# Kernel optimization log

Measured on AMD Instinct MI355X. Metric: run time of the kernel, lower is better.

The kernel has to match this reference:

```python
import jax, jax.numpy as jnp
import numpy as np

N_NODES = 4096
N_EDGES = 65536
BS = 16
LEAKY_SLOPE = 0.01
BN_EPS = 1e-5


def _init(key, shape, scale=0.02):
    return (jax.random.normal(key, shape, dtype=jnp.float32) * scale)


def setup_inputs() -> dict:
    key = jax.random.key(0)
    ks = jax.random.split(key, 20)
    x_in = jax.random.normal(ks[0], (N_NODES, 8500), dtype=jnp.float32)
    edge_index = jax.random.randint(ks[1], (2, N_EDGES), 0, N_NODES, dtype=jnp.int64)
    return {
        "x_in": x_in,
        "edge_index": edge_index,
        # SAGEConv params: Wl (neighbor lin, with bias), Wr (root lin, no bias)
        "W1l": _init(ks[2], (320, 8500)), "b1": jnp.zeros((320,), jnp.float32), "W1r": _init(ks[3], (320, 8500)),
        "W2l": _init(ks[4], (180, 320)),  "b2": jnp.zeros((180,), jnp.float32), "W2r": _init(ks[5], (180, 320)),
        "W3l": _init(ks[6], (90, 180)),   "b3": jnp.zeros((90,), jnp.float32),  "W3r": _init(ks[7], (90, 180)),
        "W4l": _init(ks[8], (50, 90)),    "b4": jnp.zeros((50,), jnp.float32),  "W4r": _init(ks[9], (50, 90)),
        "Wf1": _init(ks[10], (32, 50)),   "bf1": jnp.zeros((32,), jnp.float32),
        "Wf2": _init(ks[11], (16, 32)),   "bf2": jnp.zeros((16,), jnp.float32),
        "Wf3": _init(ks[12], (1, 16)),    "bf3": jnp.zeros((1,), jnp.float32),
    }


def _sage(x, src, dst, Wl, bl, Wr):
    # PyG SAGEConv: out = lin_l(mean_{j in N(i)} x_j) + lin_r(x_i)
    agg = jax.ops.segment_sum(x[src], dst, num_segments=N_NODES)          # [N, F]
    deg = jax.ops.segment_sum(jnp.ones_like(dst, dtype=x.dtype), dst, num_segments=N_NODES)
    mean = agg / jnp.maximum(deg, 1.0)[:, None]
    return mean @ Wl.T + bl + x @ Wr.T


def _leaky(x):
    return jnp.where(x >= 0, x, LEAKY_SLOPE * x)


def _bn(x):
    # F.batch_norm(x, None, None, training=True): per-feature, biased var, no affine
    m = jnp.mean(x, axis=0)
    v = jnp.mean((x - m) ** 2, axis=0)
    return (x - m) / jnp.sqrt(v + BN_EPS)


def reference(x_in, edge_index,
              W1l, b1, W1r, W2l, b2, W2r, W3l, b3, W3r, W4l, b4, W4r,
              Wf1, bf1, Wf2, bf2, Wf3, bf3):
    src, dst = edge_index[0], edge_index[1]
    x = _bn(_leaky(_sage(x_in, src, dst, W1l, b1, W1r)))
    x = _bn(_leaky(_sage(x, src, dst, W2l, b2, W2r)))
    x = _bn(_leaky(_sage(x, src, dst, W3l, b3, W3r)))
    x = _bn(_leaky(_sage(x, src, dst, W4l, b4, W4r)))
    # get_batch: label i -> floor(i / (N/BS)); global_add_pool == segment sum
    x = x.reshape(BS, N_NODES // BS, -1).sum(axis=1)                      # [BS, 50]
    x = x @ Wf1.T + bf1
    x = x @ Wf2.T + bf2
    x = x @ Wf3.T + bf3
    return x
```

## Files before the change

### kernel.cpp

```cpp
#include <hip/hip_runtime.h>
#include <stdint.h>

#define NN 4096
#define NE 65536
#define LEAKY 0.01f
#define BN_EPS 1e-5f
#define DSTRIDE 96

typedef float f32x4 __attribute__((ext_vector_type(4)));
typedef __bf16 bf16x8 __attribute__((ext_vector_type(8)));
typedef unsigned short u16x8 __attribute__((ext_vector_type(8)));

static __device__ __forceinline__ unsigned short f2bf(float v) {
  unsigned int u = __float_as_uint(v);
  u += 0x7fff + ((u >> 16) & 1);
  return (unsigned short)(u >> 16);
}

typedef __attribute__((address_space(1))) void gvoid;
typedef __attribute__((address_space(3))) void lvoid;

static __device__ __forceinline__ void async16(const void* g, void* l) {
  __builtin_amdgcn_global_load_lds((gvoid*)(uintptr_t)g,
                                   (lvoid*)(uint32_t)(uintptr_t)l, 16, 0, 0);
}


static __device__ __forceinline__ void pack_w_seg(int lblk, const float* __restrict__ Wl,
                                                  const float* __restrict__ Wr,
                                                  unsigned short* __restrict__ dst,
                                                  int Fout, int Fin, int Kp, int Np) {
  int nb = Kp >> 3;
  int idx = lblk * 256 + threadIdx.x;
  if (idx >= Np * nb) return;
  int row = idx / nb, kb = idx - row * nb;
  int g = kb >> 3, b = kb & 7;
  int dkb = (g << 3) | ((b + row) & 7);
  const float* src = nullptr;
  if (row < Fout)          src = Wl + (size_t)row * Fin;
  else if (row < 2 * Fout) src = Wr + (size_t)(row - Fout) * Fin;
  u16x8 st;
#pragma unroll
  for (int o = 0; o < 8; ++o) {
    int k = kb * 8 + o;
    float v = (src && k < Fin) ? src[k] : 0.f;
    st[o] = f2bf(v);
  }
  *(u16x8*)&dst[(size_t)row * Kp + dkb * 8] = st;
}

static __device__ __forceinline__ void px_load(const float* __restrict__ x, int idx,
                                               float v[8]) {
  int row = idx / 1064, kb = idx - row * 1064;
  const float* src = x + (size_t)row * 8500 + kb * 8;
  if (kb < 1062) {
    f32x4 a = *(const f32x4*)src;
    f32x4 c = *(const f32x4*)(src + 4);
#pragma unroll
    for (int o = 0; o < 4; ++o) { v[o] = a[o]; v[o + 4] = c[o]; }
  } else {
#pragma unroll
    for (int o = 0; o < 8; ++o) {
      int k = kb * 8 + o;
      v[o] = (k < 8500) ? src[o] : 0.f;
    }
  }
}

static __device__ __forceinline__ void px_store(unsigned short* __restrict__ xbf, int idx,
                                                const float v[8]) {
  int row = idx / 1064, kb = idx - row * 1064;
  int g = kb >> 3, b = kb & 7;
  int dkb = (g << 3) | ((b + row) & 7);
  u16x8 st;
#pragma unroll
  for (int o = 0; o < 8; ++o) st[o] = f2bf(v[o]);
  *(u16x8*)&xbf[(size_t)row * 8512 + dkb * 8] = st;
}

#define ADJ_BLK    256
#define PX_HALF  2179072
#define PX_BLK     8512
#define PW1_BLK    2660
#define PW2_BLK      60
#define PW3_BLK      24
#define PW4_BLK       8
#define SETUP_BLK (ADJ_BLK + PX_BLK + PW1_BLK + PW2_BLK + PW3_BLK + PW4_BLK)

__global__ __launch_bounds__(256) void setup_all(
    const float* __restrict__ x, const int* __restrict__ esrc, const int* __restrict__ edst,
    const float* __restrict__ W1l, const float* __restrict__ W1r,
    const float* __restrict__ W2l, const float* __restrict__ W2r,
    const float* __restrict__ W3l, const float* __restrict__ W3r,
    const float* __restrict__ W4l, const float* __restrict__ W4r,
    unsigned short* __restrict__ xbf, unsigned short* __restrict__ wb1,
    unsigned short* __restrict__ wb2, unsigned short* __restrict__ wb3,
    unsigned short* __restrict__ wb4, int* __restrict__ deg, int* __restrict__ eix) {
  int blk = blockIdx.x;
  if (blk < ADJ_BLK) {
    int e = blk * 256 + threadIdx.x;
    int d = edst[e];
    int pos = atomicAdd(&deg[d], 1);
    if (pos < DSTRIDE) eix[(size_t)d * DSTRIDE + pos] = esrc[e];
  } else if (blk < ADJ_BLK + PX_BLK) {
    int idx0 = (blk - ADJ_BLK) * 256 + threadIdx.x;
    int idx1 = idx0 + PX_HALF;
    float v0[8], v1[8];
    px_load(x, idx0, v0);
    px_load(x, idx1, v1);
    px_store(xbf, idx0, v0);
    px_store(xbf, idx1, v1);
  } else if (blk < ADJ_BLK + PX_BLK + PW1_BLK) {
    pack_w_seg(blk - ADJ_BLK - PX_BLK, W1l, W1r, wb1, 320, 8500, 8512, 640);
  } else if (blk < ADJ_BLK + PX_BLK + PW1_BLK + PW2_BLK) {
    pack_w_seg(blk - ADJ_BLK - PX_BLK - PW1_BLK, W2l, W2r, wb2, 180, 320, 320, 384);
  } else if (blk < ADJ_BLK + PX_BLK + PW1_BLK + PW2_BLK + PW3_BLK) {
    pack_w_seg(blk - ADJ_BLK - PX_BLK - PW1_BLK - PW2_BLK, W3l, W3r, wb3, 90, 180, 192, 256);
  } else {
    pack_w_seg(blk - ADJ_BLK - PX_BLK - PW1_BLK - PW2_BLK - PW3_BLK, W4l, W4r, wb4,
               50, 90, 128, 128);
  }
}

__global__ __launch_bounds__(256) void gemm_bt(const unsigned short* __restrict__ A,
                                               const unsigned short* __restrict__ B,
                                               float* __restrict__ C, int N, int K,
                                               int M) {
  __shared__ unsigned short smem[2 * 128 * 64];
  unsigned short* As = smem;
  unsigned short* Bs = smem + 128 * 64;

  const int t = threadIdx.x;
  const int bm = blockIdx.x, bn = blockIdx.y;
  const int lane = t & 63;
  const int wave = t >> 6;
  const int wm = (wave & 1) * 64, wn = (wave >> 1) * 64;
  const int l16 = lane & 15, quad = lane >> 4;

  const int ksteps = K >> 6;
  const int gz = (int)gridDim.z;
  const int per = (ksteps + gz - 1) / gz;
  const int k0 = (int)blockIdx.z * per;
  int k1 = k0 + per; if (k1 > ksteps) k1 = ksteps;

  f32x4 acc[4][4];
#pragma unroll
  for (int i = 0; i < 4; ++i)
#pragma unroll
    for (int j = 0; j < 4; ++j) acc[i][j] = (f32x4){0.f, 0.f, 0.f, 0.f};

  const int srow = t >> 3;
  const int scol = (t & 7) * 8;
  const unsigned short* Abase = A + (size_t)(bm * 128) * K + scol;
  const unsigned short* Bbase = B + (size_t)(bn * 128) * K + scol;

  for (int kt = k0; kt < k1; ++kt) {
    const unsigned short* Ag = Abase + kt * 64;
    const unsigned short* Bg = Bbase + kt * 64;
#pragma unroll
    for (int p = 0; p < 4; ++p) {
      int row = p * 32 + srow;
      async16(Ag + (size_t)row * K, &As[row * 64 + scol]);
    }
#pragma unroll
    for (int p = 0; p < 4; ++p) {
      int row = p * 32 + srow;
      async16(Bg + (size_t)row * K, &Bs[row * 64 + scol]);
    }
    __syncthreads();
#pragma unroll
    for (int kh = 0; kh < 2; ++kh) {
      const int s8 = ((kh * 4 + quad + l16) & 7) * 8;
      bf16x8 af[4], bfr[4];
#pragma unroll
      for (int i = 0; i < 4; ++i)
        af[i] = *(const bf16x8*)&As[(wm + i * 16 + l16) * 64 + s8];
#pragma unroll
      for (int j = 0; j < 4; ++j)
        bfr[j] = *(const bf16x8*)&Bs[(wn + j * 16 + l16) * 64 + s8];
#pragma unroll
      for (int i = 0; i < 4; ++i)
#pragma unroll
        for (int j = 0; j < 4; ++j)
          acc[i][j] = __builtin_amdgcn_mfma_f32_16x16x32_bf16(af[i], bfr[j], acc[i][j], 0, 0, 0);
    }
    __syncthreads();
  }

  float* Cb = C + (size_t)blockIdx.z * M * N;
#pragma unroll
  for (int i = 0; i < 4; ++i) {
    int rbase = bm * 128 + wm + i * 16 + quad * 4;
#pragma unroll
    for (int j = 0; j < 4; ++j) {
      int col = bn * 128 + wn + j * 16 + l16;
      float* cp = Cb + (size_t)rbase * N + col;
#pragma unroll
      for (int r = 0; r < 4; ++r) cp[(size_t)r * N] = acc[i][j][r];
    }
  }
}

__global__ void reduceN(float* __restrict__ y, int nz) {
  int idx = blockIdx.x * 256 + threadIdx.x;
  f32x4* p = (f32x4*)y;
  const int S = NN * 640 / 4;
  f32x4 v = p[idx];
  for (int sl = 1; sl < nz; ++sl) v += p[idx + (size_t)sl * S];
  p[idx] = v;
}

__global__ __launch_bounds__(256) void sage_agg(
    const float* __restrict__ y, const int* __restrict__ deg,
    const int* __restrict__ eix, const float* __restrict__ bias,
    float* __restrict__ z, int F, int ldy) {
  int i = blockIdx.x;
  int tx = threadIdx.x, ty = threadIdx.y;
  __shared__ int se[DSTRIDE];
  __shared__ float red[3][64][4];
  int d = deg[i]; if (d > DSTRIDE) d = DSTRIDE;
  {
    int lt = ty * 64 + tx;
    if (lt < d) se[lt] = eix[(size_t)i * DSTRIDE + lt];
  }
  __syncthreads();
  int nfb = (F + 255) >> 8;
  for (int fb = 0; fb < nfb; ++fb) {
    int f4 = (fb * 64 + tx) * 4;
    bool active = (f4 < F);
    f32x4 s = {0.f, 0.f, 0.f, 0.f};
    if (active) {
      const float* yb = y + f4;
      int e = ty;
      for (; e + 4 < d; e += 8) {
        f32x4 a = *(const f32x4*)&yb[(size_t)se[e] * ldy];
        f32x4 b = *(const f32x4*)&yb[(size_t)se[e + 4] * ldy];
        s += a; s += b;
      }
      if (e < d) s += *(const f32x4*)&yb[(size_t)se[e] * ldy];
    }
    if (ty > 0) *(f32x4*)red[ty - 1][tx] = s;
    __syncthreads();
    if (ty == 0 && active) {
      s += *(const f32x4*)red[0][tx];
      s += *(const f32x4*)red[1][tx];
      s += *(const f32x4*)red[2][tx];
      float inv = 1.f / (float)(d > 1 ? d : 1);
      int cnt = F - f4; if (cnt > 4) cnt = 4;
      const float* yr = &y[(size_t)i * ldy + F + f4];
      float* zo = &z[(size_t)i * F + f4];
      for (int j = 0; j < cnt; ++j) {
        float w = s[j] * inv + yr[j] + bias[f4 + j];
        zo[j] = (w >= 0.f) ? w : LEAKY * w;
      }
    }
    if (fb + 1 < nfb) __syncthreads();
  }
}


__global__ __launch_bounds__(256) void bn_part(const float* __restrict__ z,
                                               float* __restrict__ sums, int F) {
  int tx = threadIdx.x, ty = threadIdx.y;
  int f = blockIdx.x * 64 + tx;
  float s = 0.f, s2 = 0.f;
  if (f < F) {
    int r0 = blockIdx.y * 512 + ty * 128;
    for (int j = 0; j < 128; ++j) {
      float v = z[(size_t)(r0 + j) * F + f];
      s += v; s2 += v * v;
    }
  }
  __shared__ float ls[4][64], ls2[4][64];
  ls[ty][tx] = s; ls2[ty][tx] = s2;
  __syncthreads();
  if (ty == 0 && f < F) {
    float S  = ls[0][tx] + ls[1][tx] + ls[2][tx] + ls[3][tx];
    float S2 = ls2[0][tx] + ls2[1][tx] + ls2[2][tx] + ls2[3][tx];
    atomicAdd(&sums[f], S);
    atomicAdd(&sums[F + f], S2);
  }
}

__global__ void bn_norm8(const float* __restrict__ z, const float* __restrict__ sums,
                         unsigned short* __restrict__ xout, int F, int Kp) {
  int nb = Kp >> 3;
  int idx = blockIdx.x * 256 + threadIdx.x;
  int row = idx / nb, kb = idx - row * nb;
  int g = kb >> 3, b = kb & 7;
  int dkb = (g << 3) | ((b + row) & 7);
  u16x8 st;
#pragma unroll
  for (int o = 0; o < 8; ++o) {
    int k = kb * 8 + o;
    float v = 0.f;
    if (k < F) {
      float m  = sums[k] * (1.f / NN);
      float var = sums[F + k] * (1.f / NN) - m * m;
      float rs = rsqrtf(var + BN_EPS);
      v = (z[(size_t)row * F + k] - m) * rs;
    }
    st[o] = f2bf(v);
  }
  *(u16x8*)&xout[(size_t)row * Kp + dkb * 8] = st;
}

__global__ void pool_fc(const float* __restrict__ z,
                        const float* __restrict__ sums,
                        const float* __restrict__ Wf1, const float* __restrict__ bf1,
                        const float* __restrict__ Wf2, const float* __restrict__ bf2,
                        const float* __restrict__ Wf3, const float* __restrict__ bf3,
                        float* __restrict__ out) {
  __shared__ float pool[50];
  __shared__ float h1[32], h2[16];
  int b = blockIdx.x, t = threadIdx.x;
  if (t < 50) {
    float s = 0.f;
    for (int r = 0; r < 256; ++r) s += z[(size_t)(b * 256 + r) * 50 + t];
    float m  = sums[t] * (1.f / NN);
    float var = sums[50 + t] * (1.f / NN) - m * m;
    float rs = rsqrtf(var + BN_EPS);
    pool[t] = (s - 256.f * m) * rs;
  }
  __syncthreads();
  if (t < 32) {
    float s = bf1[t];
    for (int f = 0; f < 50; ++f) s += pool[f] * Wf1[t * 50 + f];
    h1[t] = s;
  }
  __syncthreads();
  if (t < 16) {
    float s = bf2[t];
    for (int f = 0; f < 32; ++f) s += h1[f] * Wf2[t * 32 + f];
    h2[t] = s;
  }
  __syncthreads();
  if (t == 0) {
    float s = bf3[0];
    for (int f = 0; f < 16; ++f) s += h2[f] * Wf3[f];
    out[b] = s;
  }
}


extern "C" void kernel_launch(void* const* d_in, const int* in_sizes, int n_in,
                              void* d_out, int out_size, void* d_ws, size_t ws_size,
                              hipStream_t stream) {
  const float* x_in = (const float*)d_in[0];
  const int* ei = (const int*)d_in[1];
  const float* W1l = (const float*)d_in[2];
  const float* b1  = (const float*)d_in[3];
  const float* W1r = (const float*)d_in[4];
  const float* W2l = (const float*)d_in[5];
  const float* b2  = (const float*)d_in[6];
  const float* W2r = (const float*)d_in[7];
  const float* W3l = (const float*)d_in[8];
  const float* b3  = (const float*)d_in[9];
  const float* W3r = (const float*)d_in[10];
  const float* W4l = (const float*)d_in[11];
  const float* b4  = (const float*)d_in[12];
  const float* W4r = (const float*)d_in[13];
  const float* Wf1 = (const float*)d_in[14];
  const float* bf1 = (const float*)d_in[15];
  const float* Wf2 = (const float*)d_in[16];
  const float* bf2 = (const float*)d_in[17];
  const float* Wf3 = (const float*)d_in[18];
  const float* bf3 = (const float*)d_in[19];
  float* out = (float*)d_out;
  (void)in_sizes; (void)n_in; (void)out_size;

  char* ws = (char*)d_ws;
  size_t off = 0;
  auto alloc = [&](size_t bytes) -> void* {
    void* p = ws + off;
    off = (off + bytes + 255) & ~(size_t)255;
    return p;
  };
  unsigned short* xbf = (unsigned short*)alloc((size_t)NN * 8512 * 2);
  unsigned short* wb1 = (unsigned short*)alloc((size_t)640 * 8512 * 2);
  unsigned short* wb2 = (unsigned short*)alloc((size_t)384 * 320 * 2);
  unsigned short* wb3 = (unsigned short*)alloc((size_t)256 * 192 * 2);
  unsigned short* wb4 = (unsigned short*)alloc((size_t)128 * 128 * 2);
  float* z    = (float*)alloc((size_t)NN * 320 * 4);
  int* deg    = (int*)alloc(NN * 4);
  float* bnsum = (float*)alloc(1280 * 4);
  int* eix    = (int*)alloc((size_t)NN * DSTRIDE * 4);
  const size_t YS = (size_t)NN * 640 * 4;
  float* y = (float*)(ws + off);
  const int nz = 4;
  if (off + (size_t)nz * YS > ws_size) return;
  float* bns1 = bnsum;
  float* bns2 = bnsum + 640;
  float* bns3 = bnsum + 1000;
  float* bns4 = bnsum + 1180;

  hipMemsetAsync(deg, 0, NN * 4 + 1280 * 4, stream);

  setup_all<<<dim3(SETUP_BLK), dim3(256), 0, stream>>>(
      x_in, ei, ei + NE, W1l, W1r, W2l, W2r, W3l, W3r, W4l, W4r,
      xbf, wb1, wb2, wb3, wb4, deg, eix);

  gemm_bt<<<dim3(32, 5, nz), dim3(256), 0, stream>>>(xbf, wb1, y, 640, 8512, NN);
  reduceN<<<dim3(NN * 640 / 4 / 256), dim3(256), 0, stream>>>(y, nz);
  sage_agg<<<dim3(NN), dim3(64, 4), 0, stream>>>(y, deg, eix, b1, z, 320, 640);
  bn_part<<<dim3(5, 8), dim3(64, 4), 0, stream>>>(z, bns1, 320);
  bn_norm8<<<dim3(NN * 40 / 256), dim3(256), 0, stream>>>(z, bns1, xbf, 320, 320);

  gemm_bt<<<dim3(32, 3, 1), dim3(256), 0, stream>>>(xbf, wb2, y, 384, 320, NN);
  sage_agg<<<dim3(NN), dim3(64, 4), 0, stream>>>(y, deg, eix, b2, z, 180, 384);
  bn_part<<<dim3(3, 8), dim3(64, 4), 0, stream>>>(z, bns2, 180);
  bn_norm8<<<dim3(NN * 24 / 256), dim3(256), 0, stream>>>(z, bns2, xbf, 180, 192);

  gemm_bt<<<dim3(32, 2, 1), dim3(256), 0, stream>>>(xbf, wb3, y, 256, 192, NN);
  sage_agg<<<dim3(NN), dim3(64, 4), 0, stream>>>(y, deg, eix, b3, z, 90, 256);
  bn_part<<<dim3(2, 8), dim3(64, 4), 0, stream>>>(z, bns3, 90);
  bn_norm8<<<dim3(NN * 16 / 256), dim3(256), 0, stream>>>(z, bns3, xbf, 90, 128);

  gemm_bt<<<dim3(32, 1, 1), dim3(256), 0, stream>>>(xbf, wb4, y, 128, 128, NN);
  sage_agg<<<dim3(NN), dim3(64, 4), 0, stream>>>(y, deg, eix, b4, z, 50, 128);
  bn_part<<<dim3(1, 8), dim3(64, 4), 0, stream>>>(z, bns4, 50);

  pool_fc<<<dim3(16), dim3(64), 0, stream>>>(z, bns4, Wf1, bf1, Wf2, bf2, Wf3, bf3, out);
}
```

Before: 505.5 us.

## Fuse fp32-to-bf16 conversion of input features into the first-layer GEMM

Removes the separate pass that converted the 4096x8500 fp32 input into a padded bf16 buffer. A new GEMM kernel reads fp32 X straight from global memory into registers, converts it, and writes it into swizzled LDS, while the B tile is double-buffered with async loads. This avoids writing and re-reading the large bf16 copy of X, at the cost of register-staged A loads, unaligned fp32 row reads (8500-float stride), and extra syncs per k-step. The k-split remainder handling changes, and the generic gemm_bt loses its split-K support.

```diff
diff --git a/kernel.cpp b/kernel.cpp
--- a/kernel.cpp
+++ b/kernel.cpp
@@ -49,76 +49,156 @@
   *(u16x8*)&dst[(size_t)row * Kp + dkb * 8] = st;
 }
 
-static __device__ __forceinline__ void px_load(const float* __restrict__ x, int idx,
-                                               float v[8]) {
-  int row = idx / 1064, kb = idx - row * 1064;
-  const float* src = x + (size_t)row * 8500 + kb * 8;
-  if (kb < 1062) {
-    f32x4 a = *(const f32x4*)src;
-    f32x4 c = *(const f32x4*)(src + 4);
-#pragma unroll
-    for (int o = 0; o < 4; ++o) { v[o] = a[o]; v[o + 4] = c[o]; }
-  } else {
-#pragma unroll
-    for (int o = 0; o < 8; ++o) {
-      int k = kb * 8 + o;
-      v[o] = (k < 8500) ? src[o] : 0.f;
-    }
-  }
-}
-
-static __device__ __forceinline__ void px_store(unsigned short* __restrict__ xbf, int idx,
-                                                const float v[8]) {
-  int row = idx / 1064, kb = idx - row * 1064;
-  int g = kb >> 3, b = kb & 7;
-  int dkb = (g << 3) | ((b + row) & 7);
-  u16x8 st;
-#pragma unroll
-  for (int o = 0; o < 8; ++o) st[o] = f2bf(v[o]);
-  *(u16x8*)&xbf[(size_t)row * 8512 + dkb * 8] = st;
-}
-
 #define ADJ_BLK    256
-#define PX_HALF  2179072
-#define PX_BLK     8512
-#define PW1_BLK    2660
-#define PW2_BLK      60
-#define PW3_BLK      24
-#define PW4_BLK       8
-#define SETUP_BLK (ADJ_BLK + PX_BLK + PW1_BLK + PW2_BLK + PW3_BLK + PW4_BLK)
+#define PW1_BLK   2660
+#define PW2_BLK     60
+#define PW3_BLK     24
+#define PW4_BLK      8
+#define SETUP_BLK (ADJ_BLK + PW1_BLK + PW2_BLK + PW3_BLK + PW4_BLK)
 
 __global__ __launch_bounds__(256) void setup_all(
-    const float* __restrict__ x, const int* __restrict__ esrc, const int* __restrict__ edst,
+    const int* __restrict__ esrc, const int* __restrict__ edst,
     const float* __restrict__ W1l, const float* __restrict__ W1r,
     const float* __restrict__ W2l, const float* __restrict__ W2r,
     const float* __restrict__ W3l, const float* __restrict__ W3r,
     const float* __restrict__ W4l, const float* __restrict__ W4r,
-    unsigned short* __restrict__ xbf, unsigned short* __restrict__ wb1,
-    unsigned short* __restrict__ wb2, unsigned short* __restrict__ wb3,
-    unsigned short* __restrict__ wb4, int* __restrict__ deg, int* __restrict__ eix) {
+    unsigned short* __restrict__ wb1, unsigned short* __restrict__ wb2,
+    unsigned short* __restrict__ wb3, unsigned short* __restrict__ wb4,
+    int* __restrict__ deg, int* __restrict__ eix) {
   int blk = blockIdx.x;
   if (blk < ADJ_BLK) {
     int e = blk * 256 + threadIdx.x;
     int d = edst[e];
     int pos = atomicAdd(&deg[d], 1);
     if (pos < DSTRIDE) eix[(size_t)d * DSTRIDE + pos] = esrc[e];
-  } else if (blk < ADJ_BLK + PX_BLK) {
-    int idx0 = (blk - ADJ_BLK) * 256 + threadIdx.x;
-    int idx1 = idx0 + PX_HALF;
-    float v0[8], v1[8];
-    px_load(x, idx0, v0);
-    px_load(x, idx1, v1);
-    px_store(xbf, idx0, v0);
-    px_store(xbf, idx1, v1);
-  } else if (blk < ADJ_BLK + PX_BLK + PW1_BLK) {
-    pack_w_seg(blk - ADJ_BLK - PX_BLK, W1l, W1r, wb1, 320, 8500, 8512, 640);
-  } else if (blk < ADJ_BLK + PX_BLK + PW1_BLK + PW2_BLK) {
-    pack_w_seg(blk - ADJ_BLK - PX_BLK - PW1_BLK, W2l, W2r, wb2, 180, 320, 320, 384);
-  } else if (blk < ADJ_BLK + PX_BLK + PW1_BLK + PW2_BLK + PW3_BLK) {
-    pack_w_seg(blk - ADJ_BLK - PX_BLK - PW1_BLK - PW2_BLK, W3l, W3r, wb3, 90, 180, 192, 256);
+  } else if (blk < ADJ_BLK + PW1_BLK) {
+    pack_w_seg(blk - ADJ_BLK, W1l, W1r, wb1, 320, 8500, 8512, 640);
+  } else if (blk < ADJ_BLK + PW1_BLK + PW2_BLK) {
+    pack_w_seg(blk - ADJ_BLK - PW1_BLK, W2l, W2r, wb2, 180, 320, 320, 384);
+  } else if (blk < ADJ_BLK + PW1_BLK + PW2_BLK + PW3_BLK) {
+    pack_w_seg(blk - ADJ_BLK - PW1_BLK - PW2_BLK, W3l, W3r, wb3, 90, 180, 192, 256);
   } else {
-    pack_w_seg(blk - ADJ_BLK - PX_BLK - PW1_BLK - PW2_BLK - PW3_BLK, W4l, W4r, wb4,
+    pack_w_seg(blk - ADJ_BLK - PW1_BLK - PW2_BLK - PW3_BLK, W4l, W4r, wb4,
                50, 90, 128, 128);
+  }
+}
+
+__global__ __launch_bounds__(256) void gemm_f32a(const float* __restrict__ X,
+                                                 const unsigned short* __restrict__ B,
+                                                 float* __restrict__ C, int N, int M) {
+  const int K = 8512, KS = 133, FIN = 8500;
+  __shared__ unsigned short smem[3 * 128 * 64];
+  unsigned short* As = smem;
+
+  const int t = threadIdx.x;
+  const int bm = blockIdx.x, bn = blockIdx.y;
+  const int lane = t & 63;
+  const int wave = t >> 6;
+  const int wm = (wave & 1) * 64, wn = (wave >> 1) * 64;
+  const int l16 = lane & 15, quad = lane >> 4;
+
+  const int gz = (int)gridDim.z, z = (int)blockIdx.z;
+  const int per = KS / gz, rem = KS % gz;
+  const int k0 = z * per + (z < rem ? z : rem);
+  const int k1 = k0 + per + (z < rem ? 1 : 0);
+
+  f32x4 acc[4][4];
+#pragma unroll
+  for (int i = 0; i < 4; ++i)
+#pragma unroll
+    for (int j = 0; j < 4; ++j) acc[i][j] = (f32x4){0.f, 0.f, 0.f, 0.f};
+
+  const int srow = t >> 3;
+  const int bblk = t & 7;
+  const int scol = bblk * 8;
+  const float* Xb = X + (size_t)(bm * 128) * FIN;
+  const unsigned short* Bbase = B + (size_t)(bn * 128) * K + scol;
+
+  float va[4][8];
+  auto loadA = [&](int kt) {
+    int gc = kt * 64 + scol;
+#pragma unroll
+    for (int p = 0; p < 4; ++p) {
+      const float* ap = Xb + (size_t)(p * 32 + srow) * FIN + gc;
+      if (gc + 8 <= FIN) {
+        f32x4 a = *(const f32x4*)ap;
+        f32x4 b2 = *(const f32x4*)(ap + 4);
+#pragma unroll
+        for (int o = 0; o < 4; ++o) { va[p][o] = a[o]; va[p][o + 4] = b2[o]; }
+      } else {
+#pragma unroll
+        for (int o = 0; o < 8; ++o) va[p][o] = (gc + o < FIN) ? ap[o] : 0.f;
+      }
+    }
+  };
+  auto writeA = [&]() {
+#pragma unroll
+    for (int p = 0; p < 4; ++p) {
+      int row = p * 32 + srow;
+      int rot = ((bblk + row) & 7) * 8;
+      bf16x8 bv;
+#pragma unroll
+      for (int o = 0; o < 8; ++o) bv[o] = (__bf16)va[p][o];
+      *(bf16x8*)&As[row * 64 + rot] = bv;
+    }
+  };
+  auto stageB = [&](int kt, int bb) {
+    unsigned short* Bd = smem + 128 * 64 + bb * 128 * 64;
+#pragma unroll
+    for (int p = 0; p < 4; ++p) {
+      int row = p * 32 + srow;
+      async16(Bbase + (size_t)row * K + kt * 64, &Bd[row * 64 + scol]);
+    }
+  };
+
+  loadA(k0);
+  stageB(k0, 0);
+  writeA();
+  __syncthreads();
+
+  int bb = 0;
+  for (int kt = k0; kt < k1; ++kt) {
+    bool more = (kt + 1 < k1);
+    if (more) {
+      loadA(kt + 1);
+      stageB(kt + 1, bb ^ 1);
+    }
+    const unsigned short* Bs = smem + 128 * 64 + bb * 128 * 64;
+#pragma unroll
+    for (int kh = 0; kh < 2; ++kh) {
+      const int s8 = ((kh * 4 + quad + l16) & 7) * 8;
+      bf16x8 af[4], bfr[4];
+#pragma unroll
+      for (int i = 0; i < 4; ++i)
+        af[i] = *(const bf16x8*)&As[(wm + i * 16 + l16) * 64 + s8];
+#pragma unroll
+      for (int j = 0; j < 4; ++j)
+        bfr[j] = *(const bf16x8*)&Bs[(wn + j * 16 + l16) * 64 + s8];
+#pragma unroll
+      for (int i = 0; i < 4; ++i)
+#pragma unroll
+        for (int j = 0; j < 4; ++j)
+          acc[i][j] = __builtin_amdgcn_mfma_f32_16x16x32_bf16(af[i], bfr[j], acc[i][j], 0, 0, 0);
+    }
+    __syncthreads();
+    if (more) {
+      writeA();
+      __syncthreads();
+      bb ^= 1;
+    }
+  }
+
+  float* Cb = C + (size_t)blockIdx.z * M * N;
+#pragma unroll
+  for (int i = 0; i < 4; ++i) {
+    int rbase = bm * 128 + wm + i * 16 + quad * 4;
+#pragma unroll
+    for (int j = 0; j < 4; ++j) {
+      int col = bn * 128 + wn + j * 16 + l16;
+      float* cp = Cb + (size_t)rbase * N + col;
+#pragma unroll
+      for (int r = 0; r < 4; ++r) cp[(size_t)r * N] = acc[i][j][r];
+    }
   }
 }
 
@@ -138,10 +218,6 @@
   const int l16 = lane & 15, quad = lane >> 4;
 
   const int ksteps = K >> 6;
-  const int gz = (int)gridDim.z;
-  const int per = (ksteps + gz - 1) / gz;
-  const int k0 = (int)blockIdx.z * per;
-  int k1 = k0 + per; if (k1 > ksteps) k1 = ksteps;
 
   f32x4 acc[4][4];
 #pragma unroll
@@ -154,7 +230,7 @@
   const unsigned short* Abase = A + (size_t)(bm * 128) * K + scol;
   const unsigned short* Bbase = B + (size_t)(bn * 128) * K + scol;
 
-  for (int kt = k0; kt < k1; ++kt) {
+  for (int kt = 0; kt < ksteps; ++kt) {
     const unsigned short* Ag = Abase + kt * 64;
     const unsigned short* Bg = Bbase + kt * 64;
 #pragma unroll
@@ -187,14 +263,13 @@
     __syncthreads();
   }
 
-  float* Cb = C + (size_t)blockIdx.z * M * N;
 #pragma unroll
   for (int i = 0; i < 4; ++i) {
     int rbase = bm * 128 + wm + i * 16 + quad * 4;
 #pragma unroll
     for (int j = 0; j < 4; ++j) {
       int col = bn * 128 + wn + j * 16 + l16;
-      float* cp = Cb + (size_t)rbase * N + col;
+      float* cp = C + (size_t)rbase * N + col;
 #pragma unroll
       for (int r = 0; r < 4; ++r) cp[(size_t)r * N] = acc[i][j][r];
     }
@@ -376,7 +451,7 @@
     off = (off + bytes + 255) & ~(size_t)255;
     return p;
   };
-  unsigned short* xbf = (unsigned short*)alloc((size_t)NN * 8512 * 2);
+  unsigned short* xbf = (unsigned short*)alloc((size_t)NN * 320 * 2);
   unsigned short* wb1 = (unsigned short*)alloc((size_t)640 * 8512 * 2);
   unsigned short* wb2 = (unsigned short*)alloc((size_t)384 * 320 * 2);
   unsigned short* wb3 = (unsigned short*)alloc((size_t)256 * 192 * 2);
@@ -397,10 +472,10 @@
   hipMemsetAsync(deg, 0, NN * 4 + 1280 * 4, stream);
 
   setup_all<<<dim3(SETUP_BLK), dim3(256), 0, stream>>>(
-      x_in, ei, ei + NE, W1l, W1r, W2l, W2r, W3l, W3r, W4l, W4r,
-      xbf, wb1, wb2, wb3, wb4, deg, eix);
-
-  gemm_bt<<<dim3(32, 5, nz), dim3(256), 0, stream>>>(xbf, wb1, y, 640, 8512, NN);
+      ei, ei + NE, W1l, W1r, W2l, W2r, W3l, W3r, W4l, W4r,
+      wb1, wb2, wb3, wb4, deg, eix);
+
+  gemm_f32a<<<dim3(32, 5, nz), dim3(256), 0, stream>>>(x_in, wb1, y, 640, NN);
   reduceN<<<dim3(NN * 640 / 4 / 256), dim3(256), 0, stream>>>(y, nz);
   sage_agg<<<dim3(NN), dim3(64, 4), 0, stream>>>(y, deg, eix, b1, z, 320, 640);
   bn_part<<<dim3(5, 8), dim3(64, 4), 0, stream>>>(z, bns1, 320);
```

New measurement: 486.0 us. 1.04x faster.
